# Kernel optimization log

Measured on AMD Instinct MI355X. Metric: run time of the kernel, lower is better.

Reference implementation:

```python
import jax, jax.numpy as jnp
import numpy as np

B, S, D, O = 8, 2048, 1024, 1024  # batch, seq_len, state_dim(=input_dim), output_dim


def setup_inputs() -> dict:
    key = jax.random.key(0)
    k_in, k_a, k_bc = jax.random.split(key, 3)
    inputs = jax.random.normal(k_in, (B, S, D), dtype=jnp.float32)
    # Stable diagonal transition (|A| < 1) so the 2048-step recurrence stays bounded.
    A = jax.random.uniform(k_a, (D,), minval=-0.99, maxval=0.99, dtype=jnp.float32)
    BC = jax.random.normal(k_bc, (D, O), dtype=jnp.float32) / D
    return {"inputs": inputs, "A": A, "BC": BC}


def reference(inputs, A, BC):
    # Diagonal LTI recurrence: h_t = A * h_{t-1} + x_t ; out_t = h_t @ BC
    # h0 = zeros (the module's h0 Parameter is initialized to zeros).
    x_tfirst = jnp.swapaxes(inputs, 0, 1)  # [S, B, D]

    def step(h, x_t):
        h = h * A + x_t
        return h, h

    h0 = jnp.zeros((inputs.shape[0], A.shape[0]), dtype=inputs.dtype)
    _, hs = jax.lax.scan(step, h0, x_tfirst)  # hs: [S, B, D]
    # Single fused projection over all timesteps instead of per-step matmuls.
    out = jnp.einsum('sbd,do->bso', hs, BC)  # [B, S, O]
    return out
```

## Files before the change

### kernel.cpp

```cpp
#include <hip/hip_runtime.h>
#include <hip/hip_bf16.h>

#define BB 8
#define SS 2048
#define DD 1024
#define OO 1024
#define MM (BB * SS)
#define KK DD
#define NN OO
#define CC 64
#define LL 32

typedef __bf16 bf16x8 __attribute__((ext_vector_type(8)));
typedef __bf16 bf16x4 __attribute__((ext_vector_type(4)));
typedef float floatx4 __attribute__((ext_vector_type(4)));

__device__ __forceinline__ float4 fma4(float4 h, float4 a, float4 v) {
    h.x = fmaf(h.x, a.x, v.x);
    h.y = fmaf(h.y, a.y, v.y);
    h.z = fmaf(h.z, a.z, v.z);
    h.w = fmaf(h.w, a.w, v.w);
    return h;
}

__global__ __launch_bounds__(256) void prep(const float* __restrict__ x,
                                            const float* __restrict__ A,
                                            float* __restrict__ carry,
                                            const float* __restrict__ BC,
                                            __bf16* __restrict__ BCt) {
    __shared__ float tile[32][33];
    const int id = blockIdx.x;
    if (id < BB * CC) {
        const int c = id & (CC - 1);
        const int b = id >> 6;
        const int i4 = threadIdx.x;
        const float4 a = ((const float4*)A)[i4];
        const float4* xp = (const float4*)(x + ((size_t)b * SS + (size_t)c * LL) * DD) + i4;
        float4 h = make_float4(0.f, 0.f, 0.f, 0.f);
#pragma unroll
        for (int t0 = 0; t0 < LL; t0 += 8) {
            float4 v[8];
#pragma unroll
            for (int u = 0; u < 8; ++u) v[u] = xp[(size_t)(t0 + u) * (DD / 4)];
#pragma unroll
            for (int u = 0; u < 8; ++u) h = fma4(h, a, v[u]);
        }
        ((float4*)carry)[((size_t)b * CC + c) * (DD / 4) + i4] = h;
    } else {
        const int t = id - BB * CC;
        const int o0 = (t & 31) * 32;
        const int d0 = (t >> 5) * 32;
        const int tx = threadIdx.x & 31;
        const int ty = threadIdx.x >> 5;
#pragma unroll
        for (int i = 0; i < 4; ++i) {
            const int dd = ty + i * 8;
            tile[dd][tx] = BC[(size_t)(d0 + dd) * OO + o0 + tx];
        }
        __syncthreads();
#pragma unroll
        for (int i = 0; i < 4; ++i) {
            const int oo = ty + i * 8;
            BCt[(size_t)(o0 + oo) * DD + d0 + tx] = (__bf16)tile[tx][oo];
        }
    }
}

__global__ __launch_bounds__(256) void scan_emit(const float* __restrict__ x,
                                                 const float* __restrict__ A,
                                                 const float* __restrict__ carry,
                                                 __bf16* __restrict__ hs) {
    const int id = blockIdx.x;
    const int c = id & (CC - 1);
    const int b = id >> 6;
    const int i4 = threadIdx.x;
    const float4 a = ((const float4*)A)[i4];
    float4 aL = a;
#pragma unroll
    for (int i = 0; i < 5; ++i) { aL.x *= aL.x; aL.y *= aL.y; aL.z *= aL.z; aL.w *= aL.w; }
    float4 h = make_float4(0.f, 0.f, 0.f, 0.f);
    const float4* cp = (const float4*)carry + (size_t)b * CC * (DD / 4) + i4;
    for (int j = 0; j < c; ++j) {
        const float4 cv = cp[(size_t)j * (DD / 4)];
        h.x = fmaf(h.x, aL.x, cv.x);
        h.y = fmaf(h.y, aL.y, cv.y);
        h.z = fmaf(h.z, aL.z, cv.z);
        h.w = fmaf(h.w, aL.w, cv.w);
    }
    const size_t base = ((size_t)b * SS + (size_t)c * LL) * DD;
    const float4* xp = (const float4*)(x + base) + i4;
    bf16x4* hp = (bf16x4*)(hs + base) + i4;
#pragma unroll
    for (int t0 = 0; t0 < LL; t0 += 8) {
        float4 v[8];
#pragma unroll
        for (int u = 0; u < 8; ++u) v[u] = xp[(size_t)(t0 + u) * (DD / 4)];
#pragma unroll
        for (int u = 0; u < 8; ++u) {
            h = fma4(h, a, v[u]);
            bf16x4 o;
            o[0] = (__bf16)h.x; o[1] = (__bf16)h.y; o[2] = (__bf16)h.z; o[3] = (__bf16)h.w;
            hp[(size_t)(t0 + u) * (DD / 4)] = o;
        }
    }
}

#define GTM 256
#define GTN 256
#define GTK 64
#define GNT (KK / GTK)

__device__ __forceinline__ void async16(void* lds, const void* g) {
    __builtin_amdgcn_global_load_lds(
        (__attribute__((address_space(1))) void*)(void*)g,
        (__attribute__((address_space(3))) void*)lds, 16, 0, 0);
}

#define MEMFENCE asm volatile("" ::: "memory")
#define BARRIER do { MEMFENCE; __builtin_amdgcn_s_barrier(); MEMFENCE; } while (0)
#define VMCNT0 asm volatile("s_waitcnt vmcnt(0)" ::: "memory")

__global__ __launch_bounds__(512, 2) void gemm_bt(const __bf16* __restrict__ Am,
                                                  const __bf16* __restrict__ Bt,
                                                  float* __restrict__ C) {
    __shared__ __align__(16) __bf16 As[2][GTM * GTK];
    __shared__ __align__(16) __bf16 Bs[2][GTN * GTK];

    const int tid = threadIdx.x;
    const int wave = tid >> 6;
    const int lane = tid & 63;
    const int wm = (wave >> 2) * 128;
    const int wn = (wave & 3) * 64;
    const int lanelo = lane & 15;
    const int quad = lane >> 4;

    const int bid = blockIdx.x;
    const int xcd = bid & 7;
    const int loc = bid >> 3;
    const int tile_m = (xcd * 8 + (loc >> 2)) * GTM;
    const int tile_n = (loc & 3) * GTN;

    const __bf16* gsrc[4][2];
    int ldsoff[4][2];
#pragma unroll
    for (int a = 0; a < 2; ++a)
#pragma unroll
        for (int u = 0; u < 2; ++u) {
            const int idx = a * 1024 + u * 512 + tid;
            const int rho = idx >> 3, qs = idx & 7;
            const int rl = rho & 127;
            const int r = (rl >> 6) * 128 + a * 64 + (rl & 63);
            const int qg = qs ^ (rho & 7);
            gsrc[a * 3][u] = Am + (size_t)(tile_m + r) * KK + qg * 8;
            ldsoff[a * 3][u] = idx * 8;
        }
#pragma unroll
    for (int b = 0; b < 2; ++b)
#pragma unroll
        for (int u = 0; u < 2; ++u) {
            const int idx = b * 1024 + u * 512 + tid;
            const int rho = idx >> 3, qs = idx & 7;
            const int rl = rho & 127;
            const int r = (rl >> 5) * 64 + b * 32 + (rl & 31);
            const int qg = qs ^ (rho & 7);
            gsrc[1 + b][u] = Bt + (size_t)(tile_n + r) * KK + qg * 8;
            ldsoff[1 + b][u] = idx * 8;
        }

    auto stage = [&](int p, int bufi, int koff) {
        __bf16* base = (p == 0 || p == 3) ? As[bufi] : Bs[bufi];
#pragma unroll
        for (int u = 0; u < 2; ++u)
            async16(base + ldsoff[p][u], gsrc[p][u] + koff);
    };

    floatx4 acc[8][4];
#pragma unroll
    for (int i = 0; i < 8; ++i)
#pragma unroll
        for (int j = 0; j < 4; ++j) acc[i][j] = (floatx4){0.f, 0.f, 0.f, 0.f};

    bf16x8 af[4][2];
    bf16x8 bv[2][2][2];

    auto read_a = [&](const __bf16* as, int mh) {
#pragma unroll
        for (int il = 0; il < 4; ++il)
#pragma unroll
            for (int kk = 0; kk < 2; ++kk) {
                const int rho = mh * 128 + (wm >> 1) + il * 16 + lanelo;
                af[il][kk] = *(const bf16x8*)(as + rho * 64 + (((kk * 4 + quad) ^ (lanelo & 7)) * 8));
            }
    };
    auto read_b = [&](const __bf16* bs, int nh) {
#pragma unroll
        for (int jl = 0; jl < 2; ++jl)
#pragma unroll
            for (int kk = 0; kk < 2; ++kk) {
                const int rho = nh * 128 + (wn >> 1) + jl * 16 + lanelo;
                bv[nh][jl][kk] = *(const bf16x8*)(bs + rho * 64 + (((kk * 4 + quad) ^ (lanelo & 7)) * 8));
            }
    };
    auto mfma16 = [&](int mh, int nh) {
        __builtin_amdgcn_s_setprio(1);
#pragma unroll
        for (int il = 0; il < 4; ++il)
#pragma unroll
            for (int jl = 0; jl < 2; ++jl)
#pragma unroll
                for (int kk = 0; kk < 2; ++kk)
                    acc[mh * 4 + il][nh * 2 + jl] = __builtin_amdgcn_mfma_f32_16x16x32_bf16(
                        af[il][kk], bv[nh][jl][kk], acc[mh * 4 + il][nh * 2 + jl], 0, 0, 0);
        __builtin_amdgcn_s_setprio(0);
    };
    auto store_q = [&](int mh, int nh) {
#pragma unroll
        for (int il = 0; il < 4; ++il) {
            const int row = tile_m + wm + (mh * 4 + il) * 16 + quad * 4;
#pragma unroll
            for (int r = 0; r < 4; ++r) {
                float* crow = C + (size_t)(row + r) * NN + tile_n + wn + lanelo;
#pragma unroll
                for (int jl = 0; jl < 2; ++jl)
                    crow[(nh * 2 + jl) * 16] = acc[mh * 4 + il][nh * 2 + jl][r];
            }
        }
    };

    stage(0, 0, 0);
    stage(3, 0, 0);
    stage(1, 0, 0);
    stage(2, 0, 0);

    for (int t = 0; t < GNT - 1; ++t) {
        const int cur = t & 1, nxt = cur ^ 1;
        const __bf16* as = As[cur];
        const __bf16* bs = Bs[cur];
        const int ko = (t + 1) * GTK;

        VMCNT0;
        BARRIER;

        stage(0, nxt, ko);
        stage(3, nxt, ko);
        stage(1, nxt, ko);
        stage(2, nxt, ko);

        read_a(as, 0);
        read_b(bs, 0);
        mfma16(0, 0);

        read_b(bs, 1);
        mfma16(0, 1);

        read_a(as, 1);
        mfma16(1, 1);

        mfma16(1, 0);
    }

    {
        const __bf16* as = As[(GNT - 1) & 1];
        const __bf16* bs = Bs[(GNT - 1) & 1];
        VMCNT0;
        BARRIER;
        read_a(as, 0);
        read_b(bs, 0);
        mfma16(0, 0);
        read_b(bs, 1);
        mfma16(0, 1);
        store_q(0, 0);
        read_a(as, 1);
        mfma16(1, 1);
        store_q(0, 1);
        mfma16(1, 0);
        store_q(1, 0);
        store_q(1, 1);
    }
}

extern "C" void kernel_launch(void* const* d_in, const int* in_sizes, int n_in,
                              void* d_out, int out_size, void* d_ws, size_t ws_size,
                              hipStream_t stream) {
    const float* x  = (const float*)d_in[0];
    const float* A  = (const float*)d_in[1];
    const float* BC = (const float*)d_in[2];
    float* out = (float*)d_out;

    char* ws = (char*)d_ws;
    __bf16* hs   = (__bf16*)ws;
    float* carry = (float*)(ws + 33554432);
    __bf16* BCt  = (__bf16*)(ws + 33554432 + 2097152);

    prep<<<dim3(BB * CC + 1024), 256, 0, stream>>>(x, A, carry, BC, BCt);
    scan_emit<<<dim3(BB * CC), 256, 0, stream>>>(x, A, carry, hs);
    gemm_bt<<<dim3(MM / GTM * (NN / GTN)), 512, 0, stream>>>(hs, BCt, out);
}
```

Baseline: 167.6 us.

## Fuse carry scan and emit into one cooperative kernel with grid sync

Merges the chunk-carry pass, the BC transpose/convert and the scan-emit pass into a single cooperative kernel separated by a grid-wide barrier. This removes one kernel launch and the gap between launches. The x chunk reloads may hit L2, since each block re-reads the same x rows right after the barrier. The cost is a cooperative launch, which requires all 512 blocks to be co-resident, plus the grid-sync overhead.

```diff
diff --git a/kernel.cpp b/kernel.cpp
--- a/kernel.cpp
+++ b/kernel.cpp
@@ -1,5 +1,8 @@
 #include <hip/hip_runtime.h>
 #include <hip/hip_bf16.h>
+#include <hip/hip_cooperative_groups.h>
+
+namespace cg = cooperative_groups;
 
 #define BB 8
 #define SS 2048
@@ -23,58 +26,59 @@
     return h;
 }
 
-__global__ __launch_bounds__(256) void prep(const float* __restrict__ x,
-                                            const float* __restrict__ A,
-                                            float* __restrict__ carry,
-                                            const float* __restrict__ BC,
-                                            __bf16* __restrict__ BCt) {
+__global__ __launch_bounds__(256) void scan_full(const float* __restrict__ x,
+                                                 const float* __restrict__ A,
+                                                 float* __restrict__ carry,
+                                                 const float* __restrict__ BC,
+                                                 __bf16* __restrict__ BCt,
+                                                 __bf16* __restrict__ hs) {
     __shared__ float tile[32][33];
-    const int id = blockIdx.x;
-    if (id < BB * CC) {
-        const int c = id & (CC - 1);
-        const int b = id >> 6;
-        const int i4 = threadIdx.x;
-        const float4 a = ((const float4*)A)[i4];
-        const float4* xp = (const float4*)(x + ((size_t)b * SS + (size_t)c * LL) * DD) + i4;
-        float4 h = make_float4(0.f, 0.f, 0.f, 0.f);
-#pragma unroll
-        for (int t0 = 0; t0 < LL; t0 += 8) {
-            float4 v[8];
-#pragma unroll
-            for (int u = 0; u < 8; ++u) v[u] = xp[(size_t)(t0 + u) * (DD / 4)];
-#pragma unroll
-            for (int u = 0; u < 8; ++u) h = fma4(h, a, v[u]);
-        }
-        ((float4*)carry)[((size_t)b * CC + c) * (DD / 4) + i4] = h;
-    } else {
-        const int t = id - BB * CC;
-        const int o0 = (t & 31) * 32;
-        const int d0 = (t >> 5) * 32;
-        const int tx = threadIdx.x & 31;
-        const int ty = threadIdx.x >> 5;
-#pragma unroll
-        for (int i = 0; i < 4; ++i) {
-            const int dd = ty + i * 8;
-            tile[dd][tx] = BC[(size_t)(d0 + dd) * OO + o0 + tx];
-        }
-        __syncthreads();
-#pragma unroll
-        for (int i = 0; i < 4; ++i) {
-            const int oo = ty + i * 8;
-            BCt[(size_t)(o0 + oo) * DD + d0 + tx] = (__bf16)tile[tx][oo];
-        }
-    }
-}
-
-__global__ __launch_bounds__(256) void scan_emit(const float* __restrict__ x,
-                                                 const float* __restrict__ A,
-                                                 const float* __restrict__ carry,
-                                                 __bf16* __restrict__ hs) {
     const int id = blockIdx.x;
     const int c = id & (CC - 1);
     const int b = id >> 6;
     const int i4 = threadIdx.x;
     const float4 a = ((const float4*)A)[i4];
+    const size_t base = ((size_t)b * SS + (size_t)c * LL) * DD;
+    const float4* xp = (const float4*)(x + base) + i4;
+
+    {
+        float4 h = make_float4(0.f, 0.f, 0.f, 0.f);
+#pragma unroll
+        for (int t0 = 0; t0 < LL; t0 += 8) {
+            float4 v[8];
+#pragma unroll
+            for (int u = 0; u < 8; ++u) v[u] = xp[(size_t)(t0 + u) * (DD / 4)];
+#pragma unroll
+            for (int u = 0; u < 8; ++u) h = fma4(h, a, v[u]);
+        }
+        ((float4*)carry)[((size_t)b * CC + c) * (DD / 4) + i4] = h;
+    }
+
+    {
+        const int tx = threadIdx.x & 31;
+        const int ty = threadIdx.x >> 5;
+#pragma unroll
+        for (int w = 0; w < 2; ++w) {
+            const int t = id * 2 + w;
+            const int o0 = (t & 31) * 32;
+            const int d0 = (t >> 5) * 32;
+            __syncthreads();
+#pragma unroll
+            for (int i = 0; i < 4; ++i) {
+                const int dd = ty + i * 8;
+                tile[dd][tx] = BC[(size_t)(d0 + dd) * OO + o0 + tx];
+            }
+            __syncthreads();
+#pragma unroll
+            for (int i = 0; i < 4; ++i) {
+                const int oo = ty + i * 8;
+                BCt[(size_t)(o0 + oo) * DD + d0 + tx] = (__bf16)tile[tx][oo];
+            }
+        }
+    }
+
+    cg::this_grid().sync();
+
     float4 aL = a;
 #pragma unroll
     for (int i = 0; i < 5; ++i) { aL.x *= aL.x; aL.y *= aL.y; aL.z *= aL.z; aL.w *= aL.w; }
@@ -87,8 +91,6 @@
         h.z = fmaf(h.z, aL.z, cv.z);
         h.w = fmaf(h.w, aL.w, cv.w);
     }
-    const size_t base = ((size_t)b * SS + (size_t)c * LL) * DD;
-    const float4* xp = (const float4*)(x + base) + i4;
     bf16x4* hp = (bf16x4*)(hs + base) + i4;
 #pragma unroll
     for (int t0 = 0; t0 < LL; t0 += 8) {
@@ -292,7 +294,8 @@
     float* carry = (float*)(ws + 33554432);
     __bf16* BCt  = (__bf16*)(ws + 33554432 + 2097152);
 
-    prep<<<dim3(BB * CC + 1024), 256, 0, stream>>>(x, A, carry, BC, BCt);
-    scan_emit<<<dim3(BB * CC), 256, 0, stream>>>(x, A, carry, hs);
+    void* args[] = {(void*)&x, (void*)&A, (void*)&carry, (void*)&BC, (void*)&BCt, (void*)&hs};
+    hipLaunchCooperativeKernel((const void*)scan_full, dim3(BB * CC), dim3(256),
+                               args, 0, stream);
     gemm_bt<<<dim3(MM / GTM * (NN / GTN)), 512, 0, stream>>>(hs, BCt, out);
 }
```

After: 238.3 us. 1.42x slower.
